# Performance work log

Hardware: AMD Instinct MI355X
Metric: run time of the kernel (lower is better)

Reference implementation:

```python
import jax, jax.numpy as jnp
import numpy as np

NUM_GROUPS = 8
EPS = 1e-5


def setup_inputs() -> dict:
    key = jax.random.key(0)
    ks = jax.random.split(key, 3)
    B, C, H, W = 32, 256, 64, 64
    x = jax.random.normal(ks[0], (B, C, H, W), dtype=jnp.float32)
    gn_weight = jnp.ones((C,), dtype=jnp.float32)
    gn_bias = jnp.zeros((C,), dtype=jnp.float32)
    # 1x1 convs stored as [out_ch, in_ch] matrices (kernel dims squeezed)
    qkv_weight = jax.random.normal(ks[1], (3 * C, C), dtype=jnp.float32) * (1.0 / np.sqrt(C))
    qkv_bias = jnp.zeros((3 * C,), dtype=jnp.float32)
    proj_weight = jax.random.normal(ks[2], (C, C), dtype=jnp.float32) * (1.0 / np.sqrt(C))
    proj_bias = jnp.zeros((C,), dtype=jnp.float32)
    return {
        "x": x,
        "gn_weight": gn_weight,
        "gn_bias": gn_bias,
        "qkv_weight": qkv_weight,
        "qkv_bias": qkv_bias,
        "proj_weight": proj_weight,
        "proj_bias": proj_bias,
    }


def _group_norm(x, weight, bias):
    B, C, H, W = x.shape
    g = x.reshape(B, NUM_GROUPS, C // NUM_GROUPS, H, W)
    mean = g.mean(axis=(2, 3, 4), keepdims=True)
    var = g.var(axis=(2, 3, 4), keepdims=True)
    g = (g - mean) * jax.lax.rsqrt(var + EPS)
    x = g.reshape(B, C, H, W)
    return x * weight[None, :, None, None] + bias[None, :, None, None]


def reference(x, gn_weight, gn_bias, qkv_weight, qkv_bias, proj_weight, proj_bias):
    B, C, H, W = x.shape
    x_norm = _group_norm(x, gn_weight, gn_bias)
    # 1x1 conv C -> 3C: contraction over channel dim
    qkv = jnp.einsum('bchw,oc->bohw', x_norm, qkv_weight) + qkv_bias[None, :, None, None]
    qkv = qkv.reshape(B, 3, C, H * W)  # [B,3,C,HW]
    q, k, v = qkv[:, 0], qkv[:, 1], qkv[:, 2]  # each [B,C,HW]
    # channel attention: attn is [B,C,C], softmax over last (key-channel) dim
    scale = 1.0 / jnp.sqrt(jnp.asarray(C, dtype=x.dtype))
    scores = jnp.einsum('bcn,bdn->bcd', q, k) * scale
    attn = jax.nn.softmax(scores, axis=-1)
    out = jnp.einsum('bcd,bdn->bcn', attn, v).reshape(B, C, H, W)
    proj = jnp.einsum('bchw,oc->bohw', out, proj_weight) + proj_bias[None, :, None, None]
    return x + proj
```

## Files before the change

kernel.cpp:

```cpp
#include <hip/hip_runtime.h>


#define B_ 32
#define C_ 256
#define N_ 4096
#define GSIZE (32 * N_)
#define EPSV 1e-5f
#define SCALE 0.0625f

#define OFF_SC    0
#define OFF_SH    8192
#define OFF_RS    16384
#define OFF_RSP   24576
#define OFF_SQP   90112
#define OFF_RALL  155648
#define OFF_UV    180224
#define OFF_CV    212992
#define OFF_CONST 221184
#define OFF_WVT   229376
#define OFF_GH    262144
#define OFF_GL    1310720
#define OFF_AT    2359296
#define OFF_S16   4456448
#define OFF_GP    5505024

typedef _Float16 half_t;
typedef half_t f16x8 __attribute__((ext_vector_type(8)));
typedef float f32x16 __attribute__((ext_vector_type(16)));

__global__ __launch_bounds__(512, 1) void gram_v4_k(const float* __restrict__ x,
                                                    float* __restrict__ ws) {
  __shared__ __align__(16) char hb[2][32768];
  int b = blockIdx.x >> 3, ks = blockIdx.x & 7;
  int t = threadIdx.x;
  const float* xb = x + (size_t)b * (C_ * (size_t)N_) + ks * 512;
  int lane = t & 63, w = t >> 6;
  int wm = w >> 2, wn = w & 3, r31 = lane & 31, hi = lane >> 5;
  int lrow = t >> 4, lc4 = t & 15;
  const float* lbase = xb + (size_t)lrow * N_ + lc4 * 4;
  f32x16 acc[4][2] = {};
  float4 stg[2][8];
  float rs[8] = {0.f, 0.f, 0.f, 0.f, 0.f, 0.f, 0.f, 0.f};
  float rq[8] = {0.f, 0.f, 0.f, 0.f, 0.f, 0.f, 0.f, 0.f};

#define LOADV(sb, c)                                                      \
  _Pragma("unroll") for (int p = 0; p < 8; ++p)                           \
      stg[sb][p] = *(const float4*)(lbase + (size_t)p * 32 * N_ + (c) * 64);

#define WRITEV(sb, buf)                                                   \
  {                                                                       \
    char* bp = hb[buf];                                                   \
    _Pragma("unroll") for (int p = 0; p < 8; ++p) {                       \
      float4 v = stg[sb][p];                                              \
      rs[p] += v.x + v.y + v.z + v.w;                                     \
      rq[p] += v.x * v.x + v.y * v.y + v.z * v.z + v.w * v.w;             \
      union { half_t h[4]; uint2 u; } H;                                  \
      H.h[0] = (half_t)v.x; H.h[1] = (half_t)v.y;                         \
      H.h[2] = (half_t)v.z; H.h[3] = (half_t)v.w;                         \
      int row = lrow + p * 32;                                            \
      int slot = (lc4 >> 1) ^ (row & 7);                                  \
      *(uint2*)(bp + row * 128 + slot * 16 + (lc4 & 1) * 8) = H.u;        \
    }                                                                     \
  }

  LOADV(0, 0);
  LOADV(1, 1);
  WRITEV(0, 0);
  __syncthreads();
  for (int c = 0; c < 8; ++c) {
    int buf = c & 1;
#pragma unroll
    for (int kk = 0; kk < 4; ++kk) {
      int kb = kk * 32 + hi * 16;
      f16x8 Af[4], Bf[2];
#pragma unroll
      for (int m = 0; m < 4; ++m) {
        int row = wm * 128 + m * 32 + r31;
        Af[m] = *(const f16x8*)(hb[buf] + row * 128 + (((kb >> 4) ^ (row & 7)) * 16));
      }
#pragma unroll
      for (int n = 0; n < 2; ++n) {
        int row = wn * 64 + n * 32 + r31;
        Bf[n] = *(const f16x8*)(hb[buf] + row * 128 + (((kb >> 4) ^ (row & 7)) * 16));
      }
#pragma unroll
      for (int m = 0; m < 4; ++m)
#pragma unroll
        for (int n = 0; n < 2; ++n)
          acc[m][n] = __builtin_amdgcn_mfma_f32_32x32x16_f16(Af[m], Bf[n], acc[m][n], 0, 0, 0);
    }
    if (c < 7) {
      int nb = (c + 1) & 1;
      WRITEV(nb, nb);
      if (c < 6) LOADV(buf, c + 2);
      __syncthreads();
    }
  }
#pragma unroll
  for (int p = 0; p < 8; ++p) {
    float s = rs[p], q = rq[p];
    s += __shfl_xor(s, 1); s += __shfl_xor(s, 2);
    s += __shfl_xor(s, 4); s += __shfl_xor(s, 8);
    q += __shfl_xor(q, 1); q += __shfl_xor(q, 2);
    q += __shfl_xor(q, 4); q += __shfl_xor(q, 8);
    if ((t & 15) == 0) {
      int row = lrow + p * 32;
      ws[OFF_RSP + (size_t)blockIdx.x * 256 + row] = s;
      ws[OFF_SQP + (size_t)blockIdx.x * 256 + row] = q;
    }
  }
  half_t* Gp = (half_t*)(ws + OFF_GP) + (size_t)blockIdx.x * 65536;
#pragma unroll
  for (int m = 0; m < 4; ++m)
#pragma unroll
    for (int n = 0; n < 2; ++n)
#pragma unroll
      for (int r = 0; r < 16; ++r) {
        int gr = wm * 128 + m * 32 + (r & 3) + 8 * (r >> 2) + 4 * hi;
        int gc = wn * 64 + n * 32 + r31;
        Gp[gr * 256 + gc] = (half_t)acc[m][n][r];
      }
#undef LOADV
#undef WRITEV
}

__global__ __launch_bounds__(256) void gsum2_k(float* __restrict__ ws) {
  int bx = blockIdx.x;
  int b = bx >> 6, seg = bx & 63;
  int e0 = seg * 1024 + threadIdx.x * 4;
  const half_t* Gp = (const half_t*)(ws + OFF_GP) + (size_t)b * 8 * 65536 + e0;
  float s[4] = {0.f, 0.f, 0.f, 0.f};
#pragma unroll
  for (int ks = 0; ks < 8; ++ks) {
    union { uint2 u; half_t h[4]; } P;
    P.u = *(const uint2*)(Gp + (size_t)ks * 65536);
#pragma unroll
    for (int i = 0; i < 4; ++i) s[i] += (float)P.h[i];
  }
  union { half_t h[4]; uint2 u; } H, L;
#pragma unroll
  for (int i = 0; i < 4; ++i) {
    H.h[i] = (half_t)s[i];
    L.h[i] = (half_t)(s[i] - (float)H.h[i]);
  }
  *(uint2*)((half_t*)(ws + OFF_GH) + (size_t)b * 65536 + e0) = H.u;
  *(uint2*)((half_t*)(ws + OFF_GL) + (size_t)b * 65536 + e0) = L.u;
}

__global__ __launch_bounds__(256) void prep2_k(const float* __restrict__ gw,
                                               const float* __restrict__ gb,
                                               const float* __restrict__ qkvw,
                                               float* __restrict__ ws) {
  int b = blockIdx.x, t = threadIdx.x;
  __shared__ float sL[256], qL[256], svecs[256], scrs[256], shsm[256];
  __shared__ float gmean[8], grstd[8];
  float s = 0.f, q = 0.f;
#pragma unroll
  for (int ks = 0; ks < 8; ++ks) {
    s += ws[OFF_RSP + (b * 8 + ks) * 256 + t];
    q += ws[OFF_SQP + (b * 8 + ks) * 256 + t];
  }
  ws[OFF_RS + b * 256 + t] = s;
  sL[t] = s; qL[t] = q;
  __syncthreads();
  if (t < 8) {
    float gs = 0.f, gq = 0.f;
    for (int i = 0; i < 32; ++i) { gs += sL[t * 32 + i]; gq += qL[t * 32 + i]; }
    float mean = gs * (1.f / GSIZE);
    float var = gq * (1.f / GSIZE) - mean * mean;
    gmean[t] = mean;
    grstd[t] = rsqrtf(var + EPSV);
  }
  __syncthreads();
  int g = t >> 5;
  float sc = grstd[g] * gw[t];
  float sh = gb[t] - gmean[g] * sc;
  ws[OFF_SC + b * 256 + t] = sc;
  ws[OFF_SH + b * 256 + t] = sh;
  svecs[t] = s * sc + 4096.f * sh;
  scrs[t] = s * sc;
  shsm[t] = sh;
  __syncthreads();
  {
    const float* r1 = qkvw + (size_t)t * 256;
    float rq = 0.f, uq = 0.f, vq = 0.f;
#pragma unroll 4
    for (int c = 0; c < 256; ++c) {
      float wv = r1[c];
      rq += wv * svecs[c]; uq += wv * scrs[c]; vq += wv * shsm[c];
    }
    ws[OFF_RALL + b * 768 + t] = rq;
    ws[OFF_UV + b * 1024 + t] = uq;
    ws[OFF_UV + b * 1024 + 256 + t] = vq;
  }
  {
    const float* r2 = qkvw + (size_t)(256 + t) * 256;
    float rk = 0.f, uk = 0.f, vk = 0.f;
#pragma unroll 4
    for (int c = 0; c < 256; ++c) {
      float wv = r2[c];
      rk += wv * svecs[c]; uk += wv * scrs[c]; vk += wv * shsm[c];
    }
    ws[OFF_RALL + b * 768 + 256 + t] = rk;
    ws[OFF_UV + b * 1024 + 512 + t] = uk;
    ws[OFF_UV + b * 1024 + 768 + t] = vk;
  }
}

__global__ __launch_bounds__(256) void wvt2_k(const float* __restrict__ qkvw,
                                              float* __restrict__ ws) {
  __shared__ float sm[64][68];
  int be = blockIdx.x * 64, bd = blockIdx.y * 64;
  int t = threadIdx.x;
#pragma unroll
  for (int i = 0; i < 4; ++i) {
    int f = t + i * 256;
    int row = f >> 4, c4 = f & 15;
    float4 v = *(const float4*)(qkvw + (size_t)(512 + bd + row) * 256 + be + c4 * 4);
    sm[row][c4 * 4 + 0] = v.x; sm[row][c4 * 4 + 1] = v.y;
    sm[row][c4 * 4 + 2] = v.z; sm[row][c4 * 4 + 3] = v.w;
  }
  __syncthreads();
  half_t* WVT = (half_t*)(ws + OFF_WVT);
#pragma unroll
  for (int i = 0; i < 4; ++i) {
    int f = t + i * 256;
    int el = f >> 4, d4 = (f & 15) * 4;
    union { half_t h[4]; uint2 u; } P;
#pragma unroll
    for (int k = 0; k < 4; ++k) P.h[k] = (half_t)sm[d4 + k][el];
    *(uint2*)(WVT + (size_t)(be + el) * 256 + bd + d4) = P.u;
  }
}

__global__ __launch_bounds__(256) void logits2_k(
    const float* __restrict__ qkvw, const float* __restrict__ qkvb,
    float* __restrict__ ws) {
  int b = blockIdx.y, r0 = blockIdx.x * 32;
  int t = threadIdx.x, lane = t & 63, w = t >> 6, r31 = lane & 31, hi = lane >> 5;
  __shared__ __align__(16) char GHL[32768];
  __shared__ __align__(16) char AHL[8192];
  __shared__ float T1s[32][257];
  __shared__ float scs[256];
  __shared__ float bk_s[256], rk_s[256], uk_s[256], vk_s[256];
  __shared__ float bq_s[32], rq_s[32], uq_s[32], vq_s[32];
  scs[t] = ws[OFF_SC + b * 256 + t];
  bk_s[t] = qkvb[256 + t];
  rk_s[t] = ws[OFF_RALL + b * 768 + 256 + t];
  uk_s[t] = ws[OFF_UV + b * 1024 + 512 + t];
  vk_s[t] = ws[OFF_UV + b * 1024 + 768 + t];
  if (t < 32) {
    bq_s[t] = qkvb[r0 + t];
    rq_s[t] = ws[OFF_RALL + b * 768 + r0 + t];
    uq_s[t] = ws[OFF_UV + b * 1024 + r0 + t];
    vq_s[t] = ws[OFF_UV + b * 1024 + 256 + r0 + t];
  }
  __syncthreads();
  const half_t* Gh = (const half_t*)(ws + OFF_GH) + (size_t)b * 65536;
  const half_t* Gl = (const half_t*)(ws + OFF_GL) + (size_t)b * 65536;
  f32x16 acc[2] = {};
  for (int k0 = 0; k0 < 256; k0 += 32) {
    {
      int row = t >> 3, c4 = t & 7;
      float4 v = *(const float4*)(qkvw + (size_t)(r0 + row) * 256 + k0 + c4 * 4);
      union { half_t h[4]; uint2 u; } H;
      H.h[0] = (half_t)(v.x * scs[k0 + c4 * 4 + 0]);
      H.h[1] = (half_t)(v.y * scs[k0 + c4 * 4 + 1]);
      H.h[2] = (half_t)(v.z * scs[k0 + c4 * 4 + 2]);
      H.h[3] = (half_t)(v.w * scs[k0 + c4 * 4 + 3]);
      int s8 = row & 7;
      *(uint2*)(AHL + row * 128 + (((c4 >> 1) ^ s8) * 16) + (c4 & 1) * 8) = H.u;
    }
    {
#pragma unroll
      for (int p = 0; p < 8; ++p) {
        int f = t + p * 256;
        int row = f >> 3, ko = f & 7;
        const half_t* src = (ko < 4) ? Gh : Gl;
        uint4 v = *(const uint4*)(src + (size_t)row * 256 + k0 + (ko & 3) * 8);
        *(uint4*)(GHL + row * 128 + ((ko ^ (row & 7)) * 16)) = v;
      }
    }
    __syncthreads();
#pragma unroll
    for (int kk = 0; kk < 2; ++kk) {
      int kb = kk * 32 + hi * 16;
      int arow = r31;
      f16x8 Aq = *(const f16x8*)(AHL + arow * 128 + (((kb >> 4) ^ (arow & 7)) * 16));
#pragma unroll
      for (int n = 0; n < 2; ++n) {
        int row = w * 64 + n * 32 + r31;
        int s8 = row & 7;
        f16x8 Bh = *(const f16x8*)(GHL + row * 128 + (((kb >> 4) ^ s8) * 16));
        f16x8 Bl = *(const f16x8*)(GHL + row * 128 + ((((kb >> 4) + 4) ^ s8) * 16));
        acc[n] = __builtin_amdgcn_mfma_f32_32x32x16_f16(Aq, Bh, acc[n], 0, 0, 0);
        acc[n] = __builtin_amdgcn_mfma_f32_32x32x16_f16(Aq, Bl, acc[n], 0, 0, 0);
      }
    }
    __syncthreads();
  }
#pragma unroll
  for (int n = 0; n < 2; ++n)
#pragma unroll
    for (int r = 0; r < 16; ++r)
      T1s[(r & 3) + 8 * (r >> 2) + 4 * hi][w * 64 + n * 32 + r31] = acc[n][r];
  __syncthreads();
  f32x16 acc2[2] = {};
  for (int k0 = 0; k0 < 256; k0 += 64) {
    {
      int row = t >> 3;
#pragma unroll
      for (int u = 0; u < 2; ++u) {
        int c4 = (t & 7) + u * 8;
        float vv[4];
#pragma unroll
        for (int j = 0; j < 4; ++j) vv[j] = T1s[row][k0 + c4 * 4 + j];
        union { half_t h[4]; uint2 u2; } H, L;
#pragma unroll
        for (int j = 0; j < 4; ++j) {
          half_t h = (half_t)vv[j];
          H.h[j] = h; L.h[j] = (half_t)(vv[j] - (float)h);
        }
        int s16 = row & 15;
        *(uint2*)(AHL + row * 256 + (((c4 >> 1) ^ s16) * 16) + (c4 & 1) * 8) = H.u2;
        *(uint2*)(AHL + row * 256 + ((((c4 >> 1) + 8) ^ s16) * 16) + (c4 & 1) * 8) = L.u2;
      }
    }
    {
#pragma unroll
      for (int p = 0; p < 16; ++p) {
        int f = t + p * 256;
        int row = f >> 4, c4 = f & 15;
        float4 v = *(const float4*)(qkvw + (size_t)(256 + row) * 256 + k0 + c4 * 4);
        union { half_t h[4]; uint2 u; } H;
        H.h[0] = (half_t)(v.x * scs[k0 + c4 * 4 + 0]);
        H.h[1] = (half_t)(v.y * scs[k0 + c4 * 4 + 1]);
        H.h[2] = (half_t)(v.z * scs[k0 + c4 * 4 + 2]);
        H.h[3] = (half_t)(v.w * scs[k0 + c4 * 4 + 3]);
        int slot = (c4 >> 1) ^ (row & 7);
        *(uint2*)(GHL + row * 128 + slot * 16 + (c4 & 1) * 8) = H.u;
      }
    }
    __syncthreads();
#pragma unroll
    for (int kk = 0; kk < 4; ++kk) {
      int kb = kk * 32 + hi * 16;
      int arow = r31;
      int s16 = arow & 15;
      f16x8 Ah = *(const f16x8*)(AHL + arow * 256 + (((kb >> 4) ^ s16) * 16));
      f16x8 Al = *(const f16x8*)(AHL + arow * 256 + ((((kb >> 4) + 8) ^ s16) * 16));
#pragma unroll
      for (int n = 0; n < 2; ++n) {
        int row = w * 64 + n * 32 + r31;
        f16x8 Bf = *(const f16x8*)(GHL + row * 128 + (((kb >> 4) ^ (row & 7)) * 16));
        acc2[n] = __builtin_amdgcn_mfma_f32_32x32x16_f16(Ah, Bf, acc2[n], 0, 0, 0);
        acc2[n] = __builtin_amdgcn_mfma_f32_32x32x16_f16(Al, Bf, acc2[n], 0, 0, 0);
      }
    }
    __syncthreads();
  }
#pragma unroll
  for (int n = 0; n < 2; ++n)
#pragma unroll
    for (int r = 0; r < 16; ++r) {
      int rr = (r & 3) + 8 * (r >> 2) + 4 * hi;
      int cc = w * 64 + n * 32 + r31;
      float v = acc2[n][r];
      float ukv = uk_s[cc] + 4096.f * vk_s[cc];
      v = (v + uq_s[rr] * vk_s[cc] + vq_s[rr] * ukv + bq_s[rr] * rk_s[cc] +
           bk_s[cc] * (rq_s[rr] + 4096.f * bq_s[rr])) * SCALE;
      T1s[rr][cc] = v;
    }
  __syncthreads();
  bk_s[t] = qkvb[512 + t];
  __syncthreads();
  {
    int row = t >> 3, ls = t & 7;
    float m = -1e30f;
#pragma unroll
    for (int i = 0; i < 32; ++i) m = fmaxf(m, T1s[row][ls + i * 8]);
    m = fmaxf(m, __shfl_xor(m, 1));
    m = fmaxf(m, __shfl_xor(m, 2));
    m = fmaxf(m, __shfl_xor(m, 4));
    float s = 0.f, cvp = 0.f;
#pragma unroll
    for (int i = 0; i < 32; ++i) {
      int col = ls + i * 8;
      float e = __expf(T1s[row][col] - m);
      T1s[row][col] = e;
      s += e;
      cvp += e * bk_s[col];
    }
    s += __shfl_xor(s, 1); s += __shfl_xor(s, 2); s += __shfl_xor(s, 4);
    cvp += __shfl_xor(cvp, 1); cvp += __shfl_xor(cvp, 2); cvp += __shfl_xor(cvp, 4);
    float inv = 1.f / s;
#pragma unroll
    for (int i = 0; i < 32; ++i) T1s[row][ls + i * 8] *= inv;
    if (ls == 0) ws[OFF_CV + b * 256 + r0 + row] = cvp * inv;
  }
  __syncthreads();
  {
    float* ATb = ws + OFF_AT + (size_t)b * 65536;
#pragma unroll
    for (int u = 0; u < 8; ++u) {
      float4 v = {T1s[u * 4 + 0][t], T1s[u * 4 + 1][t], T1s[u * 4 + 2][t],
                  T1s[u * 4 + 3][t]};
      *(float4*)(ATb + (size_t)t * 256 + r0 + u * 4) = v;
    }
  }
}

__global__ __launch_bounds__(256) void fused_s_k(const float* __restrict__ pw,
                                                 const float* __restrict__ pb,
                                                 float* __restrict__ ws) {
  int b = blockIdx.y, r0 = blockIdx.x * 32;
  int t = threadIdx.x, lane = t & 63, w = t >> 6, r31 = lane & 31, hi = lane >> 5;
  __shared__ __align__(16) char GHL[32768];
  __shared__ __align__(16) char AHL[8192];
  __shared__ float T1s[32][257];
  __shared__ float cvs[256], scv[256], shv[256];
  cvs[t] = ws[OFF_CV + b * 256 + t];
  scv[t] = ws[OFF_SC + b * 256 + t];
  shv[t] = ws[OFF_SH + b * 256 + t];
  __syncthreads();
  const float* ATb = ws + OFF_AT + (size_t)b * 65536;
  f32x16 acc[2] = {};
  for (int k0 = 0; k0 < 256; k0 += 64) {
    {
#pragma unroll
      for (int p = 0; p < 2; ++p) {
        int f = t + p * 256;
        int row = f >> 4, c4 = f & 15;
        float4 v = *(const float4*)(pw + (size_t)(r0 + row) * 256 + k0 + c4 * 4);
        union { half_t h[4]; uint2 u; } H;
        H.h[0] = (half_t)v.x; H.h[1] = (half_t)v.y;
        H.h[2] = (half_t)v.z; H.h[3] = (half_t)v.w;
        int slot = (c4 >> 1) ^ (row & 7);
        *(uint2*)(AHL + row * 128 + slot * 16 + (c4 & 1) * 8) = H.u;
      }
    }
    {
#pragma unroll
      for (int p = 0; p < 16; ++p) {
        int f = t + p * 256;
        int row = f >> 4, c4 = f & 15;
        float4 v = *(const float4*)(ATb + (size_t)row * 256 + k0 + c4 * 4);
        union { half_t h[4]; uint2 u; } H;
        H.h[0] = (half_t)v.x; H.h[1] = (half_t)v.y;
        H.h[2] = (half_t)v.z; H.h[3] = (half_t)v.w;
        int slot = (c4 >> 1) ^ (row & 7);
        *(uint2*)(GHL + row * 128 + slot * 16 + (c4 & 1) * 8) = H.u;
      }
    }
    __syncthreads();
#pragma unroll
    for (int kk = 0; kk < 4; ++kk) {
      int kb = kk * 32 + hi * 16;
      int arow = r31;
      f16x8 Af = *(const f16x8*)(AHL + arow * 128 + (((kb >> 4) ^ (arow & 7)) * 16));
#pragma unroll
      for (int n = 0; n < 2; ++n) {
        int row = w * 64 + n * 32 + r31;
        f16x8 Bf = *(const f16x8*)(GHL + row * 128 + (((kb >> 4) ^ (row & 7)) * 16));
        acc[n] = __builtin_amdgcn_mfma_f32_32x32x16_f16(Af, Bf, acc[n], 0, 0, 0);
      }
    }
    __syncthreads();
  }
#pragma unroll
  for (int n = 0; n < 2; ++n)
#pragma unroll
    for (int r = 0; r < 16; ++r)
      T1s[(r & 3) + 8 * (r >> 2) + 4 * hi][w * 64 + n * 32 + r31] = acc[n][r];
  __syncthreads();
  float cfull = 0.f;
  {
    int row = t >> 3, ls = t & 7;
    float a = 0.f;
#pragma unroll
    for (int i = 0; i < 32; ++i) {
      int c = ls + i * 8;
      a += pw[(size_t)(r0 + row) * 256 + c] * cvs[c];
    }
    a += __shfl_xor(a, 1); a += __shfl_xor(a, 2); a += __shfl_xor(a, 4);
    cfull = a + pb[r0 + row];
  }
  const half_t* WVT = (const half_t*)(ws + OFF_WVT);
  f32x16 acc2[2] = {};
  for (int k0 = 0; k0 < 256; k0 += 64) {
    {
      int row = t >> 3;
#pragma unroll
      for (int u = 0; u < 2; ++u) {
        int c4 = (t & 7) + u * 8;
        float vv[4];
#pragma unroll
        for (int j = 0; j < 4; ++j) vv[j] = T1s[row][k0 + c4 * 4 + j];
        union { half_t h[4]; uint2 u2; } H, L;
#pragma unroll
        for (int j = 0; j < 4; ++j) {
          half_t h = (half_t)vv[j];
          H.h[j] = h; L.h[j] = (half_t)(vv[j] - (float)h);
        }
        int s16 = row & 15;
        *(uint2*)(AHL + row * 256 + (((c4 >> 1) ^ s16) * 16) + (c4 & 1) * 8) = H.u2;
        *(uint2*)(AHL + row * 256 + ((((c4 >> 1) + 8) ^ s16) * 16) + (c4 & 1) * 8) = L.u2;
      }
    }
    {
#pragma unroll
      for (int p = 0; p < 8; ++p) {
        int f = t + p * 256;
        int row = f >> 3, h8 = f & 7;
        uint2 v = *(const uint2*)(WVT + (size_t)row * 256 + k0 + h8 * 8);
        uint2 v2 = *(const uint2*)(WVT + (size_t)row * 256 + k0 + h8 * 8 + 4);
        int slot = h8 ^ (row & 7);
        *(uint2*)(GHL + row * 128 + slot * 16) = v;
        *(uint2*)(GHL + row * 128 + slot * 16 + 8) = v2;
      }
    }
    __syncthreads();
#pragma unroll
    for (int kk = 0; kk < 4; ++kk) {
      int kb = kk * 32 + hi * 16;
      int arow = r31;
      int s16 = arow & 15;
      f16x8 Ah = *(const f16x8*)(AHL + arow * 256 + (((kb >> 4) ^ s16) * 16));
      f16x8 Al = *(const f16x8*)(AHL + arow * 256 + ((((kb >> 4) + 8) ^ s16) * 16));
#pragma unroll
      for (int n = 0; n < 2; ++n) {
        int row = w * 64 + n * 32 + r31;
        f16x8 Bf = *(const f16x8*)(GHL + row * 128 + (((kb >> 4) ^ (row & 7)) * 16));
        acc2[n] = __builtin_amdgcn_mfma_f32_32x32x16_f16(Ah, Bf, acc2[n], 0, 0, 0);
        acc2[n] = __builtin_amdgcn_mfma_f32_32x32x16_f16(Al, Bf, acc2[n], 0, 0, 0);
      }
    }
    __syncthreads();
  }
#pragma unroll
  for (int n = 0; n < 2; ++n)
#pragma unroll
    for (int r = 0; r < 16; ++r)
      T1s[(r & 3) + 8 * (r >> 2) + 4 * hi][w * 64 + n * 32 + r31] = acc2[n][r];
  __syncthreads();
  {
    half_t* Sb = (half_t*)(ws + OFF_S16) + (size_t)b * 65536;
    int row = t >> 3, seg = t & 7;
    float dsh = 0.f;
#pragma unroll
    for (int u = 0; u < 4; ++u) {
      union { half_t h[8]; uint4 v; } P;
#pragma unroll
      for (int j = 0; j < 8; ++j) {
        int col = seg * 32 + u * 8 + j;
        float sv = T1s[row][col];
        dsh += sv * shv[col];
        P.h[j] = (half_t)(sv * scv[col]);
      }
      *(uint4*)(Sb + (size_t)(r0 + row) * 256 + seg * 32 + u * 8) = P.v;
    }
    dsh += __shfl_xor(dsh, 1); dsh += __shfl_xor(dsh, 2); dsh += __shfl_xor(dsh, 4);
    if (seg == 0) ws[OFF_CONST + b * 256 + r0 + row] = cfull + dsh;
  }
}

__global__ __launch_bounds__(256, 4) void final_v4_k(
    const float* __restrict__ x, float* __restrict__ out,
    const float* __restrict__ ws) {
  __shared__ __align__(16) char xs[32768];
  int b = blockIdx.y, n0 = blockIdx.x * 64;
  int t = threadIdx.x, lane = t & 63, w = t >> 6;
  int r31 = lane & 31, hi = lane >> 5;
  const half_t* Sb = (const half_t*)(ws + OFF_S16) + (size_t)b * 65536;
  const float* xb = x + (size_t)b * (C_ * (size_t)N_);
  {
    int n4 = (t & 15) * 4, cb = (t >> 4) * 4;
#pragma unroll
    for (int p = 0; p < 4; ++p) {
      int c = cb + p * 64;
      float a[4][4];
#pragma unroll
      for (int i = 0; i < 4; ++i) {
        float4 v = *(const float4*)(xb + (size_t)(c + i) * N_ + n0 + n4);
        a[i][0] = v.x; a[i][1] = v.y; a[i][2] = v.z; a[i][3] = v.w;
      }
#pragma unroll
      for (int j = 0; j < 4; ++j) {
        int n = n4 + j;
        union { half_t h[4]; uint2 u; } P;
        P.h[0] = (half_t)a[0][j]; P.h[1] = (half_t)a[1][j];
        P.h[2] = (half_t)a[2][j]; P.h[3] = (half_t)a[3][j];
        int g = ((cb >> 3) & 7) ^ ((n >> 3) & 7) ^ (n & 7);
        *(uint2*)(xs + p * 8192 + n * 128 + g * 16 + (cb & 7) * 2) = P.u;
      }
    }
  }
  __syncthreads();
  f32x16 acc[2][2] = {};
  int obase = w * 64;
  const half_t* Arow0 = Sb + (size_t)(obase + r31) * 256;
  const half_t* Arow1 = Sb + (size_t)(obase + 32 + r31) * 256;
  f16x8 An0[2], An1[2];
  An0[0] = *(const f16x8*)(Arow0 + hi * 8);
  An0[1] = *(const f16x8*)(Arow1 + hi * 8);
  An1[0] = *(const f16x8*)(Arow0 + 16 + hi * 8);
  An1[1] = *(const f16x8*)(Arow1 + 16 + hi * 8);
#pragma unroll
  for (int kk = 0; kk < 16; ++kk) {
    f16x8 Af[2];
    if (kk & 1) { Af[0] = An1[0]; Af[1] = An1[1]; }
    else        { Af[0] = An0[0]; Af[1] = An0[1]; }
    if (kk < 14) {
      int ck2 = (kk + 2) * 16 + hi * 8;
      if (kk & 1) { An1[0] = *(const f16x8*)(Arow0 + ck2); An1[1] = *(const f16x8*)(Arow1 + ck2); }
      else        { An0[0] = *(const f16x8*)(Arow0 + ck2); An0[1] = *(const f16x8*)(Arow1 + ck2); }
    }
    int ck = kk * 16 + hi * 8;
    int q = ck >> 6, ch = (ck >> 3) & 7;
    f16x8 Bf[2];
#pragma unroll
    for (int n = 0; n < 2; ++n) {
      int col = n * 32 + r31;
      int g = ch ^ ((col >> 3) & 7) ^ (col & 7);
      Bf[n] = *(const f16x8*)(xs + q * 8192 + col * 128 + g * 16);
    }
#pragma unroll
    for (int m = 0; m < 2; ++m)
#pragma unroll
      for (int n = 0; n < 2; ++n)
        acc[m][n] = __builtin_amdgcn_mfma_f32_32x32x16_f16(Af[m], Bf[n], acc[m][n], 0, 0, 0);
  }
  float* ob = out + (size_t)b * (C_ * (size_t)N_);
  const float* cstb = ws + OFF_CONST + b * 256;
#pragma unroll
  for (int m = 0; m < 2; ++m)
#pragma unroll
    for (int r = 0; r < 16; ++r) {
      int o = obase + m * 32 + (r & 3) + 8 * (r >> 2) + 4 * hi;
      float cv = cstb[o];
      size_t base = (size_t)o * N_ + n0;
      int q = o >> 6, ch = (o >> 3) & 7;
#pragma unroll
      for (int n = 0; n < 2; ++n) {
        int col = n * 32 + r31;
        int g = ch ^ ((col >> 3) & 7) ^ (col & 7);
        float xr = (float)*(const half_t*)(xs + q * 8192 + col * 128 + g * 16 + (o & 7) * 2);
        ob[base + col] = acc[m][n][r] + xr + cv;
      }
    }
}

extern "C" void kernel_launch(void* const* d_in, const int* in_sizes, int n_in,
                              void* d_out, int out_size, void* d_ws,
                              size_t ws_size, hipStream_t stream) {
  const float* x = (const float*)d_in[0];
  const float* gw = (const float*)d_in[1];
  const float* gb = (const float*)d_in[2];
  const float* qkvw = (const float*)d_in[3];
  const float* qkvb = (const float*)d_in[4];
  const float* pw = (const float*)d_in[5];
  const float* pb = (const float*)d_in[6];
  float* out = (float*)d_out;
  float* ws = (float*)d_ws;

  hipLaunchKernelGGL(gram_v4_k, dim3(256), dim3(512), 0, stream, x, ws);
  hipLaunchKernelGGL(prep2_k, dim3(32), dim3(256), 0, stream, gw, gb, qkvw, ws);
  hipLaunchKernelGGL(gsum2_k, dim3(2048), dim3(256), 0, stream, ws);
  hipLaunchKernelGGL(wvt2_k, dim3(4, 4), dim3(256), 0, stream, qkvw, ws);
  hipLaunchKernelGGL(logits2_k, dim3(8, 32), dim3(256), 0, stream, qkvw, qkvb, ws);
  hipLaunchKernelGGL(fused_s_k, dim3(8, 32), dim3(256), 0, stream, pw, pb, ws);
  hipLaunchKernelGGL(final_v4_k, dim3(64, 32), dim3(256), 0, stream, x, out, ws);
}
```

Before: 212.0 us.

## Split Gram kernel output columns across four blocks to raise occupancy

```diff
diff --git a/kernel.cpp b/kernel.cpp
--- a/kernel.cpp
+++ b/kernel.cpp
@@ -28,100 +28,98 @@
 typedef half_t f16x8 __attribute__((ext_vector_type(8)));
 typedef float f32x16 __attribute__((ext_vector_type(16)));
 
-__global__ __launch_bounds__(512, 1) void gram_v4_k(const float* __restrict__ x,
-                                                    float* __restrict__ ws) {
-  __shared__ __align__(16) char hb[2][32768];
-  int b = blockIdx.x >> 3, ks = blockIdx.x & 7;
+__global__ __launch_bounds__(256) void gram_v5_k(const float* __restrict__ x,
+                                                 float* __restrict__ ws) {
+  __shared__ __align__(16) char hb[2][16384];
+  int bid = blockIdx.x;
+  int slice = bid & 255, q = bid >> 8;
+  int b = slice >> 3, ks = slice & 7;
   int t = threadIdx.x;
   const float* xb = x + (size_t)b * (C_ * (size_t)N_) + ks * 512;
   int lane = t & 63, w = t >> 6;
-  int wm = w >> 2, wn = w & 3, r31 = lane & 31, hi = lane >> 5;
-  int lrow = t >> 4, lc4 = t & 15;
+  int r31 = lane & 31, hi = lane >> 5;
+  int lrow = t >> 3, lc4 = t & 7;
   const float* lbase = xb + (size_t)lrow * N_ + lc4 * 4;
-  f32x16 acc[4][2] = {};
-  float4 stg[2][8];
+  f32x16 acc[2][2] = {};
+  float4 stg[8];
   float rs[8] = {0.f, 0.f, 0.f, 0.f, 0.f, 0.f, 0.f, 0.f};
   float rq[8] = {0.f, 0.f, 0.f, 0.f, 0.f, 0.f, 0.f, 0.f};
 
-#define LOADV(sb, c)                                                      \
+#define G5_LOAD(c)                                                        \
   _Pragma("unroll") for (int p = 0; p < 8; ++p)                           \
-      stg[sb][p] = *(const float4*)(lbase + (size_t)p * 32 * N_ + (c) * 64);
-
-#define WRITEV(sb, buf)                                                   \
+      stg[p] = *(const float4*)(lbase + (size_t)p * 32 * N_ + (c) * 32);
+
+#define G5_WRITE(buf)                                                     \
   {                                                                       \
     char* bp = hb[buf];                                                   \
     _Pragma("unroll") for (int p = 0; p < 8; ++p) {                       \
-      float4 v = stg[sb][p];                                              \
+      float4 v = stg[p];                                                  \
       rs[p] += v.x + v.y + v.z + v.w;                                     \
       rq[p] += v.x * v.x + v.y * v.y + v.z * v.z + v.w * v.w;             \
       union { half_t h[4]; uint2 u; } H;                                  \
       H.h[0] = (half_t)v.x; H.h[1] = (half_t)v.y;                         \
       H.h[2] = (half_t)v.z; H.h[3] = (half_t)v.w;                         \
       int row = lrow + p * 32;                                            \
-      int slot = (lc4 >> 1) ^ (row & 7);                                  \
-      *(uint2*)(bp + row * 128 + slot * 16 + (lc4 & 1) * 8) = H.u;        \
+      int g = (lc4 >> 1) ^ (row & 3);                                     \
+      *(uint2*)(bp + row * 64 + g * 16 + (lc4 & 1) * 8) = H.u;            \
     }                                                                     \
   }
 
-  LOADV(0, 0);
-  LOADV(1, 1);
-  WRITEV(0, 0);
-  __syncthreads();
-  for (int c = 0; c < 8; ++c) {
-    int buf = c & 1;
-#pragma unroll
-    for (int kk = 0; kk < 4; ++kk) {
-      int kb = kk * 32 + hi * 16;
-      f16x8 Af[4], Bf[2];
-#pragma unroll
-      for (int m = 0; m < 4; ++m) {
-        int row = wm * 128 + m * 32 + r31;
-        Af[m] = *(const f16x8*)(hb[buf] + row * 128 + (((kb >> 4) ^ (row & 7)) * 16));
+  G5_LOAD(0);
+  G5_WRITE(0);
+  __syncthreads();
+  for (int c = 0; c < 16; ++c) {
+    if (c < 15) G5_LOAD(c + 1);
+    const char* bp = hb[c & 1];
+#pragma unroll
+    for (int kk = 0; kk < 2; ++kk) {
+      int g4 = kk * 2 + hi;
+      f16x8 Af[2], Bf[2];
+#pragma unroll
+      for (int m = 0; m < 2; ++m) {
+        int row = w * 64 + m * 32 + r31;
+        Af[m] = *(const f16x8*)(bp + row * 64 + ((g4 ^ (row & 3)) * 16));
       }
 #pragma unroll
       for (int n = 0; n < 2; ++n) {
-        int row = wn * 64 + n * 32 + r31;
-        Bf[n] = *(const f16x8*)(hb[buf] + row * 128 + (((kb >> 4) ^ (row & 7)) * 16));
-      }
-#pragma unroll
-      for (int m = 0; m < 4; ++m)
+        int row = q * 64 + n * 32 + r31;
+        Bf[n] = *(const f16x8*)(bp + row * 64 + ((g4 ^ (row & 3)) * 16));
+      }
+#pragma unroll
+      for (int m = 0; m < 2; ++m)
 #pragma unroll
         for (int n = 0; n < 2; ++n)
           acc[m][n] = __builtin_amdgcn_mfma_f32_32x32x16_f16(Af[m], Bf[n], acc[m][n], 0, 0, 0);
     }
-    if (c < 7) {
-      int nb = (c + 1) & 1;
-      WRITEV(nb, nb);
-      if (c < 6) LOADV(buf, c + 2);
-      __syncthreads();
-    }
-  }
-#pragma unroll
-  for (int p = 0; p < 8; ++p) {
-    float s = rs[p], q = rq[p];
-    s += __shfl_xor(s, 1); s += __shfl_xor(s, 2);
-    s += __shfl_xor(s, 4); s += __shfl_xor(s, 8);
-    q += __shfl_xor(q, 1); q += __shfl_xor(q, 2);
-    q += __shfl_xor(q, 4); q += __shfl_xor(q, 8);
-    if ((t & 15) == 0) {
-      int row = lrow + p * 32;
-      ws[OFF_RSP + (size_t)blockIdx.x * 256 + row] = s;
-      ws[OFF_SQP + (size_t)blockIdx.x * 256 + row] = q;
-    }
-  }
-  half_t* Gp = (half_t*)(ws + OFF_GP) + (size_t)blockIdx.x * 65536;
-#pragma unroll
-  for (int m = 0; m < 4; ++m)
+    if (c < 15) G5_WRITE((c + 1) & 1);
+    __syncthreads();
+  }
+  if (q == 0) {
+#pragma unroll
+    for (int p = 0; p < 8; ++p) {
+      float s = rs[p], qq = rq[p];
+      s += __shfl_xor(s, 1); s += __shfl_xor(s, 2); s += __shfl_xor(s, 4);
+      qq += __shfl_xor(qq, 1); qq += __shfl_xor(qq, 2); qq += __shfl_xor(qq, 4);
+      if ((t & 7) == 0) {
+        int row = lrow + p * 32;
+        ws[OFF_RSP + (size_t)slice * 256 + row] = s;
+        ws[OFF_SQP + (size_t)slice * 256 + row] = qq;
+      }
+    }
+  }
+  half_t* Gp = (half_t*)(ws + OFF_GP) + (size_t)slice * 65536;
+#pragma unroll
+  for (int m = 0; m < 2; ++m)
 #pragma unroll
     for (int n = 0; n < 2; ++n)
 #pragma unroll
       for (int r = 0; r < 16; ++r) {
-        int gr = wm * 128 + m * 32 + (r & 3) + 8 * (r >> 2) + 4 * hi;
-        int gc = wn * 64 + n * 32 + r31;
+        int gr = w * 64 + m * 32 + (r & 3) + 8 * (r >> 2) + 4 * hi;
+        int gc = q * 64 + n * 32 + r31;
         Gp[gr * 256 + gc] = (half_t)acc[m][n][r];
       }
-#undef LOADV
-#undef WRITEV
+#undef G5_LOAD
+#undef G5_WRITE
 }
 
 __global__ __launch_bounds__(256) void gsum2_k(float* __restrict__ ws) {
@@ -663,7 +661,7 @@
   float* out = (float*)d_out;
   float* ws = (float*)d_ws;
 
-  hipLaunchKernelGGL(gram_v4_k, dim3(256), dim3(512), 0, stream, x, ws);
+  hipLaunchKernelGGL(gram_v5_k, dim3(1024), dim3(256), 0, stream, x, ws);
   hipLaunchKernelGGL(prep2_k, dim3(32), dim3(256), 0, stream, gw, gb, qkvw, ws);
   hipLaunchKernelGGL(gsum2_k, dim3(2048), dim3(256), 0, stream, ws);
   hipLaunchKernelGGL(wvt2_k, dim3(4, 4), dim3(256), 0, stream, qkvw, ws);
```

New measurement: 219.1 us. +3.3%, slower.
